# Kernel optimization log

Measured on AMD Instinct MI355X. Metric: run time of the kernel, lower is better.

The kernel has to match this reference:

```python
import jax, jax.numpy as jnp
import numpy as np

D = 1024   # dims
H = 16     # heads
HD = D // H  # head_dim = 64
F = HD // 2  # rotary frequency count


def _layernorm(x, g, b, eps=1e-5):
    m = x.mean(-1, keepdims=True)
    v = jnp.mean((x - m) ** 2, axis=-1, keepdims=True)
    return (x - m) * jax.lax.rsqrt(v + eps) * g + b


def _freq_base():
    # mask=None branch of rotary._compute_freqs: mel-style frequencies
    mel_max = 2595.0 * np.log10(1.0 + 4000.0 / 200.0)
    scale = 10.0 ** (np.linspace(0.0, mel_max, F) / 2595.0) - 1.0
    return jnp.asarray(200.0 * scale / 1000.0, dtype=jnp.float32)  # [F]


def _rope_polar(xh, radius, theta):
    # xh: [b,h,c,hd]; radius: [b,c] (learned per-token magnitude); theta: [c,F]
    # complex multiply of interleaved pairs by r*exp(i*theta)
    b_, h_, c_, hd_ = xh.shape
    xp = xh.reshape(b_, h_, c_, F, 2)
    xr, xi = xp[..., 0], xp[..., 1]
    cos = jnp.cos(theta)[None, None]  # [1,1,c,F]
    sin = jnp.sin(theta)[None, None]
    r = radius[:, None, :, None]      # [b,1,c,1]
    out_r = r * (xr * cos - xi * sin)
    out_i = r * (xr * sin + xi * cos)
    return jnp.stack([out_r, out_i], axis=-1).reshape(b_, h_, c_, hd_)


def setup_inputs() -> dict:
    key = jax.random.key(0)
    ks = jax.random.split(key, 6)
    B, C = 2, 2048
    s = 0.02
    return {
        "x": jax.random.normal(ks[0], (B, C, D), jnp.float32),
        "ln_q_g": jnp.ones((D,), jnp.float32),
        "ln_q_b": jnp.zeros((D,), jnp.float32),
        "Wq": jax.random.normal(ks[1], (D, D), jnp.float32) * s,
        "bq": jnp.zeros((D,), jnp.float32),
        "ln_kv_g": jnp.ones((D,), jnp.float32),
        "ln_kv_b": jnp.zeros((D,), jnp.float32),
        "Wkv": jax.random.normal(ks[2], (D, 2 * D), jnp.float32) * s,
        "bkv": jnp.zeros((2 * D,), jnp.float32),
        "Wout": jax.random.normal(ks[3], (D, D), jnp.float32) * s,
        "bout": jnp.zeros((D,), jnp.float32),
        "lnh_g": jnp.ones((HD,), jnp.float32),
        "lnh_b": jnp.zeros((HD,), jnp.float32),
        "Wr": jax.random.normal(ks[4], (D, 1), jnp.float32) * s,
        "br": jnp.zeros((1,), jnp.float32),
    }


def reference(x, ln_q_g, ln_q_b, Wq, bq, ln_kv_g, ln_kv_b, Wkv, bkv,
              Wout, bout, lnh_g, lnh_b, Wr, br):
    B, C, _ = x.shape
    # q path: norm -> linear -> [b,h,c,d]
    q = (_layernorm(x, ln_q_g, ln_q_b) @ Wq + bq).reshape(B, C, H, HD).transpose(0, 2, 1, 3)
    # kv path: norm -> linear -> [2,b,h,c,d]
    kv = (_layernorm(x, ln_kv_g, ln_kv_b) @ Wkv + bkv).reshape(B, C, 2, H, HD).transpose(2, 0, 3, 1, 4)
    k, v = kv[0], kv[1]
    # polar RoPE with learned per-token radius (xa = x for both q and k)
    t = jnp.arange(C, dtype=jnp.float32)
    theta = t[:, None] * _freq_base()[None, :]               # [C,F]
    per_step = (x @ Wr + br)[..., 0]                         # [B,C]
    radius = jnp.clip(per_step / 100.0, 0.5, 2.0)
    q = _rope_polar(q, radius, theta)
    k = _rope_polar(k, radius, theta)
    # per-head LayerNorm fused into SDPA inputs
    qn = _layernorm(q, lnh_g, lnh_b)
    kn = _layernorm(k, lnh_g, lnh_b)
    # non-causal SDPA (torch default scale = 1/sqrt(head_dim))
    logits = jnp.einsum('bhqd,bhkd->bhqk', qn, kn) / jnp.sqrt(jnp.float32(HD))
    attn = jax.nn.softmax(logits, axis=-1)
    o = jnp.einsum('bhqk,bhkd->bhqd', attn, v)
    o = o.transpose(0, 2, 1, 3).reshape(B, C, D)
    return o @ Wout + bout
```

## Files before the change

kernel.cpp:

```cpp
#include <hip/hip_runtime.h>
#include <math.h>

#define D_MODEL 1024
#define NHEADS  16
#define HEADD   64
#define NFREQ   32
#define BATCH   2
#define CSEQ    2048
#define NROWS   (BATCH*CSEQ)
#define NQKV    (3*D_MODEL)

typedef _Float16 half8  __attribute__((ext_vector_type(8)));
typedef _Float16 half4v __attribute__((ext_vector_type(4)));
typedef float    f32x4  __attribute__((ext_vector_type(4)));

__device__ __forceinline__ void async16(void* lds, const void* g)
{
    __builtin_amdgcn_global_load_lds((const __attribute__((address_space(1))) unsigned int*)g,
                                     (__attribute__((address_space(3))) unsigned int*)lds,
                                     16, 0, 0);
}

__global__ __launch_bounds__(256) void build_cs_kernel(float2* __restrict__ cs)
{
    int i = blockIdx.x * 256 + threadIdx.x;
    if (i >= CSEQ * NFREQ) return;
    int c = i >> 5, f = i & (NFREQ - 1);
    double mel_max = 2595.0 * log10(21.0);
    double step    = mel_max / (double)(NFREQ - 1);
    double freq    = 200.0 * (pow(10.0, step * (double)f / 2595.0) - 1.0) / 1000.0;
    float fr = (float)freq;
    float th = (float)c * fr;
    float s, co;
    sincosf(th, &s, &co);
    cs[i] = make_float2(co, s);
}

__global__ __launch_bounds__(256) void bias_init_kernel(
    const float* __restrict__ bq, const float* __restrict__ bkv, float* __restrict__ be)
{
    int i = blockIdx.x * 256 + threadIdx.x;
    if (i < D_MODEL) be[i] = bq[i];
    else if (i < NQKV) be[i] = bkv[i - D_MODEL];
}

__global__ __launch_bounds__(256) void transpose_fold_kernel(
    const float* __restrict__ in, _Float16* __restrict__ out, int R, int C,
    int rowoff, const float* __restrict__ scale,
    const float* __restrict__ bfold, float* __restrict__ bias_acc)
{
    __shared__ float t[32][33];
    __shared__ float part[4][32];
    int bx = blockIdx.x * 32;
    int by = blockIdx.y * 32;
    int tx = threadIdx.x, ty = threadIdx.y;
    #pragma unroll
    for (int i = ty; i < 32; i += 8)
        t[i][tx] = in[(size_t)(by + i) * C + bx + tx];
    __syncthreads();
    float sc = scale ? scale[by + tx] : 1.f;
    #pragma unroll
    for (int i = ty; i < 32; i += 8)
        out[(size_t)(rowoff + bx + i) * R + by + tx] = (_Float16)(t[tx][i] * sc);
    if (bfold) {
        float p = 0.f;
        #pragma unroll
        for (int i = ty; i < 32; i += 8)
            p += bfold[by + i] * t[i][tx];
        p += __shfl_xor(p, 32);
        if ((ty & 1) == 0) part[ty >> 1][tx] = p;
        __syncthreads();
        if (ty == 0)
            atomicAdd(&bias_acc[rowoff + bx + tx],
                      part[0][tx] + part[1][tx] + part[2][tx] + part[3][tx]);
    }
}

__global__ __launch_bounds__(256) void ln_radius_kernel(
    const float* __restrict__ x,
    const float* __restrict__ Wr,  const float* __restrict__ br,
    _Float16* __restrict__ xn, float* __restrict__ radius)
{
    int row = blockIdx.x;
    int tid = threadIdx.x;
    float4 xv = ((const float4*)(x + (size_t)row * D_MODEL))[tid];
    float4 wv = ((const float4*)Wr)[tid];
    float s  = xv.x + xv.y + xv.z + xv.w;
    float ss = xv.x*xv.x + xv.y*xv.y + xv.z*xv.z + xv.w*xv.w;
    float dr = xv.x*wv.x + xv.y*wv.y + xv.z*wv.z + xv.w*wv.w;
    #pragma unroll
    for (int off = 1; off < 64; off <<= 1) {
        s  += __shfl_xor(s, off);
        ss += __shfl_xor(ss, off);
        dr += __shfl_xor(dr, off);
    }
    __shared__ float red[3][4];
    int w = tid >> 6, lane = tid & 63;
    if (lane == 0) { red[0][w] = s; red[1][w] = ss; red[2][w] = dr; }
    __syncthreads();
    s  = red[0][0] + red[0][1] + red[0][2] + red[0][3];
    ss = red[1][0] + red[1][1] + red[1][2] + red[1][3];
    float mean = s * (1.f / D_MODEL);
    float var  = ss * (1.f / D_MODEL) - mean * mean;
    float rinv = rsqrtf(var + 1e-5f);
    half4v o4 = { (_Float16)((xv.x - mean) * rinv), (_Float16)((xv.y - mean) * rinv),
                  (_Float16)((xv.z - mean) * rinv), (_Float16)((xv.w - mean) * rinv) };
    *(half4v*)&xn[(size_t)row * D_MODEL + tid * 4] = o4;
    if (tid == 0) {
        float drt = red[2][0] + red[2][1] + red[2][2] + red[2][3];
        float p = (drt + br[0]) * 0.01f;
        radius[row] = fminf(fmaxf(p, 0.5f), 2.0f);
    }
}

__device__ __forceinline__ void gemm_core32(
    const _Float16* __restrict__ A, const _Float16* __restrict__ B,
    int bm, int bn, int K, _Float16* As, _Float16* Bs, f32x4 (*acc)[4])
{
    int tid = threadIdx.x, lane = tid & 63, w = tid >> 6;
    int wm = w >> 1, wn = w & 1;
    int l15 = lane & 15, lg = lane >> 4;
    int sr  = lane >> 2;
    int sch = lane & 3;

    auto stage = [&](int buf, int k0) {
        #pragma unroll
        for (int i = 0; i < 2; ++i) {
            int seg = w * 2 + i;
            int row = seg * 16 + sr;
            async16(&As[buf * 4096 + seg * 512], &A[(size_t)(bm + row) * K + k0 + sch * 8]);
            async16(&Bs[buf * 4096 + seg * 512], &B[(size_t)(bn + row) * K + k0 + sch * 8]);
        }
    };

    stage(0, 0);
    __syncthreads();
    int cur = 0;
    for (int k0 = 0; k0 < K; k0 += 32) {
        if (k0 + 32 < K) stage(cur ^ 1, k0 + 32);
        half8 af[4], bf[4];
        #pragma unroll
        for (int m = 0; m < 4; ++m)
            af[m] = *(const half8*)&As[cur * 4096 + (wm * 64 + m * 16 + l15) * 32 + lg * 8];
        #pragma unroll
        for (int n = 0; n < 4; ++n)
            bf[n] = *(const half8*)&Bs[cur * 4096 + (wn * 64 + n * 16 + l15) * 32 + lg * 8];
        #pragma unroll
        for (int m = 0; m < 4; ++m)
            #pragma unroll
            for (int n = 0; n < 4; ++n)
                acc[m][n] = __builtin_amdgcn_mfma_f32_16x16x32_f16(af[m], bf[n], acc[m][n], 0, 0, 0);
        __syncthreads();
        cur ^= 1;
    }
}

__global__ __launch_bounds__(256, 4) void gemm_qkv_kernel(
    const _Float16* __restrict__ xn,  const _Float16* __restrict__ WT,
    const float* __restrict__ bias_eff,
    const float* __restrict__ radius, const float2* __restrict__ cs_tab,
    const float* __restrict__ lnh_g,  const float* __restrict__ lnh_b,
    _Float16* __restrict__ qn, _Float16* __restrict__ kn, _Float16* __restrict__ vT)
{
    __shared__ _Float16 As[2 * 4096];
    __shared__ _Float16 Bs[2 * 4096];
    int orig = blockIdx.x;
    int wg = (orig & 7) * 96 + (orig >> 3);
    int bm = (wg / 24) * 128;
    int bn = (wg % 24) * 128;

    f32x4 acc[4][4];
    f32x4 z = {0.f, 0.f, 0.f, 0.f};
    #pragma unroll
    for (int m = 0; m < 4; ++m)
        #pragma unroll
        for (int n = 0; n < 4; ++n) acc[m][n] = z;

    gemm_core32(xn, WT, bm, bn, D_MODEL, As, Bs, acc);

    int tid = threadIdx.x, lane = tid & 63, w = tid >> 6;
    int wm = w >> 1, wn = w & 1;
    int l15 = lane & 15, lg = lane >> 4;
    int colbase = bn + wn * 64;

    float bb4[4];
    #pragma unroll
    for (int n = 0; n < 4; ++n) bb4[n] = bias_eff[colbase + n * 16 + l15];

    if (colbase >= 2 * D_MODEL) {
        int vcolb = colbase - 2 * D_MODEL;
        int h = vcolb >> 6;
        #pragma unroll
        for (int m = 0; m < 4; ++m) {
            int row0 = bm + wm * 64 + m * 16 + lg * 4;
            int b = row0 >> 11, c = row0 & (CSEQ - 1);
            #pragma unroll
            for (int n = 0; n < 4; ++n) {
                int d = n * 16 + l15;
                half4v v4 = { (_Float16)(acc[m][n][0] + bb4[n]),
                              (_Float16)(acc[m][n][1] + bb4[n]),
                              (_Float16)(acc[m][n][2] + bb4[n]),
                              (_Float16)(acc[m][n][3] + bb4[n]) };
                *(half4v*)&vT[((size_t)(b * NHEADS + h) * HEADD + d) * CSEQ + c] = v4;
            }
        }
        return;
    }

    bool isq = colbase < D_MODEL;
    int h = (colbase & (D_MODEL - 1)) >> 6;
    _Float16* dst = isq ? qn : kn;
    float qs = isq ? 0.125f : 1.f;
    bool im = (l15 & 1) != 0;

    float g4[4], bh4[4];
    #pragma unroll
    for (int n = 0; n < 4; ++n) {
        g4[n]  = lnh_g[n * 16 + l15];
        bh4[n] = lnh_b[n * 16 + l15];
    }

    #pragma unroll
    for (int m = 0; m < 4; ++m)
        #pragma unroll
        for (int r = 0; r < 4; ++r) {
            int row = bm + wm * 64 + m * 16 + lg * 4 + r;
            int b = row >> 11, c = row & (CSEQ - 1);
            float rr = radius[row];
            float vals[4];
            float s = 0.f, ss = 0.f;
            #pragma unroll
            for (int n = 0; n < 4; ++n) {
                float v0 = acc[m][n][r] + bb4[n];
                float pr = __shfl_xor(v0, 1);
                float2 cs = cs_tab[c * NFREQ + ((n * 16 + l15) >> 1)];
                float xr_ = im ? pr : v0;
                float xi_ = im ? v0 : pr;
                float rot = im ? rr * (xr_ * cs.y + xi_ * cs.x)
                               : rr * (xr_ * cs.x - xi_ * cs.y);
                vals[n] = rot;
                s += rot; ss += rot * rot;
            }
            #pragma unroll
            for (int off = 1; off < 16; off <<= 1) {
                s  += __shfl_xor(s, off);
                ss += __shfl_xor(ss, off);
            }
            float mean = s * (1.f / 64.f);
            float var  = ss * (1.f / 64.f) - mean * mean;
            float ri   = rsqrtf(var + 1e-5f);
            size_t base = ((size_t)(b * NHEADS + h) * CSEQ + c) * HEADD;
            #pragma unroll
            for (int n = 0; n < 4; ++n) {
                float o = ((vals[n] - mean) * ri * g4[n] + bh4[n]) * qs;
                dst[base + n * 16 + l15] = (_Float16)o;
            }
        }
}

__global__ __launch_bounds__(256, 4) void gemm_out_kernel(
    const _Float16* __restrict__ A, const _Float16* __restrict__ BT,
    const float* __restrict__ bias, float* __restrict__ C)
{
    __shared__ _Float16 As[2 * 4096];
    __shared__ _Float16 Bs[2 * 4096];
    int orig = blockIdx.x;
    int wg = (orig & 7) * 32 + (orig >> 3);
    int bm = (wg >> 3) * 128;
    int bn = (wg & 7) * 128;

    f32x4 acc[4][4];
    f32x4 z = {0.f, 0.f, 0.f, 0.f};
    #pragma unroll
    for (int m = 0; m < 4; ++m)
        #pragma unroll
        for (int n = 0; n < 4; ++n) acc[m][n] = z;

    gemm_core32(A, BT, bm, bn, D_MODEL, As, Bs, acc);

    int tid = threadIdx.x, lane = tid & 63, w = tid >> 6;
    int wm = w >> 1, wn = w & 1;
    int l15 = lane & 15, lg = lane >> 4;
    #pragma unroll
    for (int m = 0; m < 4; ++m) {
        int row = bm + wm * 64 + m * 16 + lg * 4;
        #pragma unroll
        for (int n = 0; n < 4; ++n) {
            int col = bn + wn * 64 + n * 16 + l15;
            float bb = bias[col];
            #pragma unroll
            for (int r = 0; r < 4; ++r)
                C[(size_t)(row + r) * D_MODEL + col] = acc[m][n][r] + bb;
        }
    }
}

#define KVB 64
#define NT  (CSEQ / KVB)

__global__ __launch_bounds__(256, 4) void attn_kernel(
    const _Float16* __restrict__ qn, const _Float16* __restrict__ kn,
    const _Float16* __restrict__ vT, _Float16* __restrict__ o)
{
    __shared__ _Float16 KsB[2][KVB * 64];
    __shared__ _Float16 VsB[2][KVB * 64];
    __shared__ _Float16 P[4][16 * 64];
    int tid = threadIdx.x, lane = tid & 63, w = tid >> 6;
    int l15 = lane & 15, lg = lane >> 4;

    int orig = blockIdx.x;
    int wg   = (orig & 7) * 128 + (orig >> 3);
    int bh   = wg >> 5;
    int qc   = wg & 31;
    int q0   = qc * 64 + w * 16;

    const _Float16* qh = qn + (size_t)bh * CSEQ * HEADD;
    const _Float16* kh = kn + (size_t)bh * CSEQ * HEADD;
    const _Float16* vh = vT + (size_t)bh * HEADD * CSEQ;

    half8 aq[2];
    #pragma unroll
    for (int ks = 0; ks < 2; ++ks)
        aq[ks] = *(const half8*)&qh[(size_t)(q0 + l15) * HEADD + ks * 32 + lg * 8];

    f32x4 z = {0.f, 0.f, 0.f, 0.f};
    f32x4 oacc[4];
    #pragma unroll
    for (int d4 = 0; d4 < 4; ++d4) oacc[d4] = z;
    float mrun = -1e30f, lrun = 0.f;

    int srow_in = lane >> 3;
    int csrc    = (lane & 7) ^ srow_in;
    int lsw     = l15 & 7;

    auto stage = [&](int buf, int kt) {
        int k0 = kt * KVB;
        #pragma unroll
        for (int i = 0; i < 2; ++i) {
            int seg = w * 2 + i;
            int r = seg * 8 + srow_in;
            async16(&KsB[buf][seg * 512], &kh[(size_t)(k0 + r) * HEADD + csrc * 8]);
            async16(&VsB[buf][seg * 512], &vh[(size_t)r * CSEQ + k0 + csrc * 8]);
        }
    };

    stage(0, 0);
    __syncthreads();
    int cur = 0;

    for (int kt = 0; kt < NT; ++kt) {
        if (kt + 1 < NT) stage(cur ^ 1, kt + 1);

        f32x4 st[4];
        #pragma unroll
        for (int n = 0; n < 4; ++n) st[n] = z;
        #pragma unroll
        for (int ks = 0; ks < 2; ++ks) {
            half8 ak[4];
            #pragma unroll
            for (int n = 0; n < 4; ++n) {
                int row = n * 16 + l15;
                int ch = (ks * 4 + lg) ^ (row & 7);
                ak[n] = *(const half8*)&KsB[cur][row * 64 + ch * 8];
            }
            #pragma unroll
            for (int n = 0; n < 4; ++n)
                st[n] = __builtin_amdgcn_mfma_f32_16x16x32_f16(ak[n], aq[ks], st[n], 0, 0, 0);
        }

        float mx0 = fmaxf(fmaxf(st[0][0], st[0][1]), fmaxf(st[0][2], st[0][3]));
        float mx1 = fmaxf(fmaxf(st[1][0], st[1][1]), fmaxf(st[1][2], st[1][3]));
        float mx2 = fmaxf(fmaxf(st[2][0], st[2][1]), fmaxf(st[2][2], st[2][3]));
        float mx3 = fmaxf(fmaxf(st[3][0], st[3][1]), fmaxf(st[3][2], st[3][3]));
        float tmax = fmaxf(fmaxf(mx0, mx1), fmaxf(mx2, mx3));
        tmax = fmaxf(tmax, __shfl_xor(tmax, 16));
        tmax = fmaxf(tmax, __shfl_xor(tmax, 32));

        if (!__all(tmax <= mrun + 8.f)) {
            float nm = fmaxf(mrun, tmax);
            float sc = __expf(mrun - nm);
            mrun = nm;
            lrun *= sc;
            float scO[4];
            #pragma unroll
            for (int r = 0; r < 4; ++r) scO[r] = __shfl(sc, lg * 4 + r);
            #pragma unroll
            for (int d4 = 0; d4 < 4; ++d4)
                #pragma unroll
                for (int r = 0; r < 4; ++r) oacc[d4][r] *= scO[r];
        }

        float ps = 0.f;
        #pragma unroll
        for (int n = 0; n < 4; ++n)
            #pragma unroll
            for (int r = 0; r < 4; ++r) {
                float e = __expf(st[n][r] - mrun);
                st[n][r] = e;
                ps += e;
            }
        ps += __shfl_xor(ps, 16);
        ps += __shfl_xor(ps, 32);
        lrun += ps;

        #pragma unroll
        for (int n = 0; n < 4; ++n) {
            half4v pk;
            #pragma unroll
            for (int r = 0; r < 4; ++r) pk[r] = (_Float16)st[n][r];
            int t  = n * 2 + (lg >> 1);
            int tp = t ^ lsw;
            *(half4v*)&P[w][l15 * 64 + tp * 8 + (lg & 1) * 4] = pk;
        }

        #pragma unroll
        for (int ks = 0; ks < 2; ++ks) {
            int tp2 = (ks * 4 + lg) ^ lsw;
            half8 ap = *(const half8*)&P[w][l15 * 64 + tp2 * 8];
            half8 bv[4];
            #pragma unroll
            for (int d4 = 0; d4 < 4; ++d4) {
                int row = d4 * 16 + l15;
                int ch = (ks * 4 + lg) ^ (row & 7);
                bv[d4] = *(const half8*)&VsB[cur][row * 64 + ch * 8];
            }
            #pragma unroll
            for (int d4 = 0; d4 < 4; ++d4)
                oacc[d4] = __builtin_amdgcn_mfma_f32_16x16x32_f16(ap, bv[d4], oacc[d4], 0, 0, 0);
        }

        __syncthreads();
        cur ^= 1;
    }

    int b = bh >> 4, h = bh & 15;
    #pragma unroll
    for (int r = 0; r < 4; ++r) {
        float lr = __shfl(lrun, lg * 4 + r);
        float inv = 1.f / lr;
        int c = q0 + lg * 4 + r;
        size_t base = ((size_t)b * CSEQ + c) * D_MODEL + h * HEADD;
        #pragma unroll
        for (int d4 = 0; d4 < 4; ++d4)
            o[base + d4 * 16 + l15] = (_Float16)(oacc[d4][r] * inv);
    }
}

extern "C" void kernel_launch(void* const* d_in, const int* in_sizes, int n_in,
                              void* d_out, int out_size, void* d_ws, size_t ws_size,
                              hipStream_t stream)
{
    (void)in_sizes; (void)n_in; (void)out_size; (void)ws_size;
    const float* x      = (const float*)d_in[0];
    const float* ln_q_g = (const float*)d_in[1];
    const float* ln_q_b = (const float*)d_in[2];
    const float* Wq     = (const float*)d_in[3];
    const float* bq     = (const float*)d_in[4];
    const float* ln_kv_g= (const float*)d_in[5];
    const float* ln_kv_b= (const float*)d_in[6];
    const float* Wkv    = (const float*)d_in[7];
    const float* bkv    = (const float*)d_in[8];
    const float* Wout   = (const float*)d_in[9];
    const float* bout   = (const float*)d_in[10];
    const float* lnh_g  = (const float*)d_in[11];
    const float* lnh_b  = (const float*)d_in[12];
    const float* Wr     = (const float*)d_in[13];
    const float* br     = (const float*)d_in[14];
    float* out = (float*)d_out;

    char* ws = (char*)d_ws;
    size_t off = 0;
    auto alloc = [&](size_t bytes) -> void* {
        void* p = ws + off;
        off += (bytes + 255) & ~(size_t)255;
        return p;
    };
    _Float16* WqkvT  = (_Float16*)alloc((size_t)NQKV * D_MODEL * 2);
    _Float16* WoutT  = (_Float16*)alloc((size_t)D_MODEL * D_MODEL * 2);
    float*    bias_e = (float*)   alloc((size_t)NQKV * 4);
    float*    radius = (float*)   alloc((size_t)NROWS * 4);
    float2*   cs_tab = (float2*)  alloc((size_t)CSEQ * NFREQ * 8);
    _Float16* vT     = (_Float16*)alloc((size_t)BATCH * NHEADS * HEADD * CSEQ * 2);
    _Float16* xn     = (_Float16*)alloc((size_t)NROWS * D_MODEL * 2);
    _Float16* qn     = (_Float16*)alloc((size_t)NROWS * D_MODEL * 2);
    _Float16* kn     = (_Float16*)alloc((size_t)NROWS * D_MODEL * 2);
    _Float16* o_h    = (_Float16*)alloc((size_t)NROWS * D_MODEL * 2);

    hipLaunchKernelGGL(bias_init_kernel, dim3(NQKV / 256), dim3(256), 0, stream, bq, bkv, bias_e);
    hipLaunchKernelGGL(build_cs_kernel, dim3(CSEQ * NFREQ / 256), dim3(256), 0, stream, cs_tab);
    hipLaunchKernelGGL(transpose_fold_kernel, dim3(D_MODEL/32, D_MODEL/32), dim3(32, 8), 0, stream,
                       Wq, WqkvT, D_MODEL, D_MODEL, 0, ln_q_g, ln_q_b, bias_e);
    hipLaunchKernelGGL(transpose_fold_kernel, dim3(2*D_MODEL/32, D_MODEL/32), dim3(32, 8), 0, stream,
                       Wkv, WqkvT, D_MODEL, 2*D_MODEL, D_MODEL, ln_kv_g, ln_kv_b, bias_e);
    hipLaunchKernelGGL(transpose_fold_kernel, dim3(D_MODEL/32, D_MODEL/32), dim3(32, 8), 0, stream,
                       Wout, WoutT, D_MODEL, D_MODEL, 0, (const float*)nullptr,
                       (const float*)nullptr, (float*)nullptr);
    hipLaunchKernelGGL(ln_radius_kernel, dim3(NROWS), dim3(256), 0, stream,
                       x, Wr, br, xn, radius);
    hipLaunchKernelGGL(gemm_qkv_kernel, dim3(768), dim3(256), 0, stream,
                       xn, WqkvT, bias_e, radius, cs_tab, lnh_g, lnh_b, qn, kn, vT);
    hipLaunchKernelGGL(attn_kernel, dim3(BATCH*NHEADS*CSEQ/64), dim3(256), 0, stream,
                       qn, kn, vT, o_h);
    hipLaunchKernelGGL(gemm_out_kernel, dim3(256), dim3(256), 0, stream,
                       o_h, WoutT, bout, out);
}
```

Baseline: 153.6 us.

## Triple-buffer GEMM LDS pipeline and merge prep kernels into fewer launches

The GEMM core moves from a double-buffered loop with two barriers per k-step to a three-stage ring. Loads are issued two tiles ahead, and explicit vmcnt waits plus a single barrier per iteration let global-to-LDS copies overlap more MFMA work. Occupancy hints drop from 4 to 3 blocks per CU because LDS use grows. Separately, the five small prep launches (bias init, cos/sin table, three weight transposes) are merged into two kernels to cut launch overhead.

After: 150.0 us. 1.02x faster.

```diff
diff --git a/kernel.cpp b/kernel.cpp
--- a/kernel.cpp
+++ b/kernel.cpp
@@ -21,52 +21,73 @@
                                      16, 0, 0);
 }
 
-__global__ __launch_bounds__(256) void build_cs_kernel(float2* __restrict__ cs)
-{
-    int i = blockIdx.x * 256 + threadIdx.x;
-    if (i >= CSEQ * NFREQ) return;
-    int c = i >> 5, f = i & (NFREQ - 1);
-    double mel_max = 2595.0 * log10(21.0);
-    double step    = mel_max / (double)(NFREQ - 1);
-    double freq    = 200.0 * (pow(10.0, step * (double)f / 2595.0) - 1.0) / 1000.0;
-    float fr = (float)freq;
-    float th = (float)c * fr;
-    float s, co;
-    sincosf(th, &s, &co);
-    cs[i] = make_float2(co, s);
-}
-
-__global__ __launch_bounds__(256) void bias_init_kernel(
+__global__ __launch_bounds__(256) void prep_misc_kernel(
+    float2* __restrict__ cs,
     const float* __restrict__ bq, const float* __restrict__ bkv, float* __restrict__ be)
 {
-    int i = blockIdx.x * 256 + threadIdx.x;
-    if (i < D_MODEL) be[i] = bq[i];
-    else if (i < NQKV) be[i] = bkv[i - D_MODEL];
-}
-
-__global__ __launch_bounds__(256) void transpose_fold_kernel(
-    const float* __restrict__ in, _Float16* __restrict__ out, int R, int C,
-    int rowoff, const float* __restrict__ scale,
-    const float* __restrict__ bfold, float* __restrict__ bias_acc)
-{
-    __shared__ float t[32][33];
+    int bid = blockIdx.x;
+    int tid = threadIdx.x;
+    if (bid < 256) {
+        int i = bid * 256 + tid;
+        int c = i >> 5, f = i & (NFREQ - 1);
+        double mel_max = 2595.0 * log10(21.0);
+        double step    = mel_max / (double)(NFREQ - 1);
+        double freq    = 200.0 * (pow(10.0, step * (double)f / 2595.0) - 1.0) / 1000.0;
+        float fr = (float)freq;
+        float th = (float)c * fr;
+        float s, co;
+        sincosf(th, &s, &co);
+        cs[i] = make_float2(co, s);
+    } else {
+        int i = (bid - 256) * 256 + tid;
+        if (i < D_MODEL) be[i] = bq[i];
+        else if (i < NQKV) be[i] = bkv[i - D_MODEL];
+    }
+}
+
+__global__ void transpose_all_kernel(
+    const float* __restrict__ Wq,  const float* __restrict__ Wkv,
+    const float* __restrict__ Wout,
+    const float* __restrict__ gq,  const float* __restrict__ bqf,
+    const float* __restrict__ gkv, const float* __restrict__ bkvf,
+    _Float16* __restrict__ WqkvT, _Float16* __restrict__ WoutT,
+    float* __restrict__ bias_acc)
+{
+    const float* in; _Float16* out; int R, C, rowoff;
+    const float* scale; const float* bfold;
+    int id = blockIdx.x, bx, by;
+    if (id < 1024) {
+        in = Wq; out = WqkvT; R = D_MODEL; C = D_MODEL; rowoff = 0;
+        scale = gq; bfold = bqf;
+        bx = (id & 31) * 32; by = (id >> 5) * 32;
+    } else if (id < 3072) {
+        int t = id - 1024;
+        in = Wkv; out = WqkvT; R = D_MODEL; C = 2 * D_MODEL; rowoff = D_MODEL;
+        scale = gkv; bfold = bkvf;
+        bx = (t & 63) * 32; by = (t >> 6) * 32;
+    } else {
+        int t = id - 3072;
+        in = Wout; out = WoutT; R = D_MODEL; C = D_MODEL; rowoff = 0;
+        scale = nullptr; bfold = nullptr;
+        bx = (t & 31) * 32; by = (t >> 5) * 32;
+    }
+
+    __shared__ float tb[32][33];
     __shared__ float part[4][32];
-    int bx = blockIdx.x * 32;
-    int by = blockIdx.y * 32;
     int tx = threadIdx.x, ty = threadIdx.y;
     #pragma unroll
     for (int i = ty; i < 32; i += 8)
-        t[i][tx] = in[(size_t)(by + i) * C + bx + tx];
+        tb[i][tx] = in[(size_t)(by + i) * C + bx + tx];
     __syncthreads();
     float sc = scale ? scale[by + tx] : 1.f;
     #pragma unroll
     for (int i = ty; i < 32; i += 8)
-        out[(size_t)(rowoff + bx + i) * R + by + tx] = (_Float16)(t[tx][i] * sc);
+        out[(size_t)(rowoff + bx + i) * R + by + tx] = (_Float16)(tb[tx][i] * sc);
     if (bfold) {
         float p = 0.f;
         #pragma unroll
         for (int i = ty; i < 32; i += 8)
-            p += bfold[by + i] * t[i][tx];
+            p += bfold[by + i] * tb[i][tx];
         p += __shfl_xor(p, 32);
         if ((ty & 1) == 0) part[ty >> 1][tx] = p;
         __syncthreads();
@@ -113,7 +134,7 @@
     }
 }
 
-__device__ __forceinline__ void gemm_core32(
+__device__ __forceinline__ void gemm_core32p(
     const _Float16* __restrict__ A, const _Float16* __restrict__ B,
     int bm, int bn, int K, _Float16* As, _Float16* Bs, f32x4 (*acc)[4])
 {
@@ -133,37 +154,44 @@
         }
     };
 
+    int nt = K >> 5;
     stage(0, 0);
-    __syncthreads();
-    int cur = 0;
-    for (int k0 = 0; k0 < K; k0 += 32) {
-        if (k0 + 32 < K) stage(cur ^ 1, k0 + 32);
+    stage(1, 32);
+
+    for (int t = 0; t < nt; ++t) {
+        if (t + 1 < nt) asm volatile("s_waitcnt vmcnt(4)" ::: "memory");
+        else            asm volatile("s_waitcnt vmcnt(0)" ::: "memory");
+        __builtin_amdgcn_sched_barrier(0);
+        __builtin_amdgcn_s_barrier();
+        __builtin_amdgcn_sched_barrier(0);
+        if (t + 2 < nt) stage((t + 2) % 3, (t + 2) << 5);
+
+        const _Float16* Ab = &As[(t % 3) * 4096];
+        const _Float16* Bb = &Bs[(t % 3) * 4096];
         half8 af[4], bf[4];
         #pragma unroll
         for (int m = 0; m < 4; ++m)
-            af[m] = *(const half8*)&As[cur * 4096 + (wm * 64 + m * 16 + l15) * 32 + lg * 8];
+            af[m] = *(const half8*)&Ab[(wm * 64 + m * 16 + l15) * 32 + lg * 8];
         #pragma unroll
         for (int n = 0; n < 4; ++n)
-            bf[n] = *(const half8*)&Bs[cur * 4096 + (wn * 64 + n * 16 + l15) * 32 + lg * 8];
+            bf[n] = *(const half8*)&Bb[(wn * 64 + n * 16 + l15) * 32 + lg * 8];
         #pragma unroll
         for (int m = 0; m < 4; ++m)
             #pragma unroll
             for (int n = 0; n < 4; ++n)
                 acc[m][n] = __builtin_amdgcn_mfma_f32_16x16x32_f16(af[m], bf[n], acc[m][n], 0, 0, 0);
-        __syncthreads();
-        cur ^= 1;
-    }
-}
-
-__global__ __launch_bounds__(256, 4) void gemm_qkv_kernel(
+    }
+}
+
+__global__ __launch_bounds__(256, 3) void gemm_qkv_kernel(
     const _Float16* __restrict__ xn,  const _Float16* __restrict__ WT,
     const float* __restrict__ bias_eff,
     const float* __restrict__ radius, const float2* __restrict__ cs_tab,
     const float* __restrict__ lnh_g,  const float* __restrict__ lnh_b,
     _Float16* __restrict__ qn, _Float16* __restrict__ kn, _Float16* __restrict__ vT)
 {
-    __shared__ _Float16 As[2 * 4096];
-    __shared__ _Float16 Bs[2 * 4096];
+    __shared__ _Float16 As[3 * 4096];
+    __shared__ _Float16 Bs[3 * 4096];
     int orig = blockIdx.x;
     int wg = (orig & 7) * 96 + (orig >> 3);
     int bm = (wg / 24) * 128;
@@ -176,7 +204,7 @@
         #pragma unroll
         for (int n = 0; n < 4; ++n) acc[m][n] = z;
 
-    gemm_core32(xn, WT, bm, bn, D_MODEL, As, Bs, acc);
+    gemm_core32p(xn, WT, bm, bn, D_MODEL, As, Bs, acc);
 
     int tid = threadIdx.x, lane = tid & 63, w = tid >> 6;
     int wm = w >> 1, wn = w & 1;
@@ -258,12 +286,12 @@
         }
 }
 
-__global__ __launch_bounds__(256, 4) void gemm_out_kernel(
+__global__ __launch_bounds__(256, 3) void gemm_out_kernel(
     const _Float16* __restrict__ A, const _Float16* __restrict__ BT,
     const float* __restrict__ bias, float* __restrict__ C)
 {
-    __shared__ _Float16 As[2 * 4096];
-    __shared__ _Float16 Bs[2 * 4096];
+    __shared__ _Float16 As[3 * 4096];
+    __shared__ _Float16 Bs[3 * 4096];
     int orig = blockIdx.x;
     int wg = (orig & 7) * 32 + (orig >> 3);
     int bm = (wg >> 3) * 128;
@@ -276,7 +304,7 @@
         #pragma unroll
         for (int n = 0; n < 4; ++n) acc[m][n] = z;
 
-    gemm_core32(A, BT, bm, bn, D_MODEL, As, Bs, acc);
+    gemm_core32p(A, BT, bm, bn, D_MODEL, As, Bs, acc);
 
     int tid = threadIdx.x, lane = tid & 63, w = tid >> 6;
     int wm = w >> 1, wn = w & 1;
@@ -486,15 +514,11 @@
     _Float16* kn     = (_Float16*)alloc((size_t)NROWS * D_MODEL * 2);
     _Float16* o_h    = (_Float16*)alloc((size_t)NROWS * D_MODEL * 2);
 
-    hipLaunchKernelGGL(bias_init_kernel, dim3(NQKV / 256), dim3(256), 0, stream, bq, bkv, bias_e);
-    hipLaunchKernelGGL(build_cs_kernel, dim3(CSEQ * NFREQ / 256), dim3(256), 0, stream, cs_tab);
-    hipLaunchKernelGGL(transpose_fold_kernel, dim3(D_MODEL/32, D_MODEL/32), dim3(32, 8), 0, stream,
-                       Wq, WqkvT, D_MODEL, D_MODEL, 0, ln_q_g, ln_q_b, bias_e);
-    hipLaunchKernelGGL(transpose_fold_kernel, dim3(2*D_MODEL/32, D_MODEL/32), dim3(32, 8), 0, stream,
-                       Wkv, WqkvT, D_MODEL, 2*D_MODEL, D_MODEL, ln_kv_g, ln_kv_b, bias_e);
-    hipLaunchKernelGGL(transpose_fold_kernel, dim3(D_MODEL/32, D_MODEL/32), dim3(32, 8), 0, stream,
-                       Wout, WoutT, D_MODEL, D_MODEL, 0, (const float*)nullptr,
-                       (const float*)nullptr, (float*)nullptr);
+    hipLaunchKernelGGL(prep_misc_kernel, dim3(268), dim3(256), 0, stream,
+                       cs_tab, bq, bkv, bias_e);
+    hipLaunchKernelGGL(transpose_all_kernel, dim3(4096), dim3(32, 8), 0, stream,
+                       Wq, Wkv, Wout, ln_q_g, ln_q_b, ln_kv_g, ln_kv_b,
+                       WqkvT, WoutT, bias_e);
     hipLaunchKernelGGL(ln_radius_kernel, dim3(NROWS), dim3(256), 0, stream,
                        x, Wr, br, xn, radius);
     hipLaunchKernelGGL(gemm_qkv_kernel, dim3(768), dim3(256), 0, stream,
```
